# Kernel optimization log

Measured on AMD Instinct MI355X. Metric: run time of the kernel, lower is better.

## Reference

```python
import jax, jax.numpy as jnp
import numpy as np

HEADS = 4
EPS = 1e-5

def _layernorm(x, g, b):
    mu = jnp.mean(x, axis=-1, keepdims=True)
    var = jnp.var(x, axis=-1, keepdims=True)
    return (x - mu) / jnp.sqrt(var + EPS) * g + b

def setup_inputs() -> dict:
    key = jax.random.key(0)
    ks = jax.random.split(key, 16)
    N, dim, k, G = 400000, 256, 1, 4096
    h = jax.random.normal(ks[0], (N, dim), dtype=jnp.float32)
    batch = jnp.sort(jax.random.randint(ks[1], (N,), 0, G).astype(jnp.int64))
    s = 1.0 / np.sqrt(dim)
    return {
        "h": h,
        "batch": batch,
        "num_graphs": G,
        "seed": jax.random.normal(ks[2], (k, dim), dtype=jnp.float32),
        "in_proj_w": jax.random.uniform(ks[3], (3 * dim, dim), minval=-s, maxval=s, dtype=jnp.float32),
        "in_proj_b": jnp.zeros((3 * dim,), jnp.float32),
        "out_w": jax.random.uniform(ks[4], (dim, dim), minval=-s, maxval=s, dtype=jnp.float32),
        "out_b": jnp.zeros((dim,), jnp.float32),
        "w1": jax.random.uniform(ks[5], (4 * dim, dim), minval=-s, maxval=s, dtype=jnp.float32),
        "b1": jnp.zeros((4 * dim,), jnp.float32),
        "w2": jax.random.uniform(ks[6], (dim, 4 * dim), minval=-1.0 / np.sqrt(4 * dim), maxval=1.0 / np.sqrt(4 * dim), dtype=jnp.float32),
        "b2": jnp.zeros((dim,), jnp.float32),
        "g1": jnp.ones((dim,), jnp.float32),
        "beta1": jnp.zeros((dim,), jnp.float32),
        "g2": jnp.ones((dim,), jnp.float32),
        "beta2": jnp.zeros((dim,), jnp.float32),
    }

def reference(h, batch, num_graphs, seed, in_proj_w, in_proj_b, out_w, out_b,
              w1, b1, w2, b2, g1, beta1, g2, beta2):
    N, dim = h.shape
    k = seed.shape[0]
    hd = dim // HEADS
    G = num_graphs
    # q/k/v projections (torch MHA packed in_proj: rows [0:dim]=Q, [dim:2dim]=K, [2dim:]=V)
    q = seed @ in_proj_w[:dim].T + in_proj_b[:dim]                 # [k, dim]
    kk = h @ in_proj_w[dim:2 * dim].T + in_proj_b[dim:2 * dim]     # [N, dim]
    vv = h @ in_proj_w[2 * dim:].T + in_proj_b[2 * dim:]           # [N, dim]
    qh = q.reshape(k, HEADS, hd).transpose(1, 0, 2)                # [H, k, hd]
    kh = kk.reshape(N, HEADS, hd)                                  # [N, H, hd]
    vh = vv.reshape(N, HEADS, hd)                                  # [N, H, hd]
    scale = 1.0 / np.sqrt(hd)
    scores = jnp.einsum('hkd,nhd->nhk', qh, kh) * scale            # [N, H, k]
    # segment softmax over nodes of each graph
    smax = jax.ops.segment_max(scores, batch, num_segments=G)      # [G, H, k]
    e = jnp.exp(scores - smax[batch])                              # [N, H, k]
    denom = jax.ops.segment_sum(e, batch, num_segments=G)          # [G, H, k]
    wv = jax.ops.segment_sum(e[:, :, :, None] * vh[:, :, None, :], batch, num_segments=G)  # [G, H, k, hd]
    attn = jnp.where(denom[..., None] > 0, wv / jnp.maximum(denom, 1e-9)[..., None], 0.0)
    attn = attn.transpose(0, 2, 1, 3).reshape(G, k, dim)           # [G, k, dim]
    o = attn @ out_w.T + out_b                                     # [G, k, dim]
    x = _layernorm(o + seed[None, :, :], g1, beta1)
    f = jax.nn.relu(x @ w1.T + b1) @ w2.T + b2
    x = _layernorm(x + f, g2, beta2)
    # empty graphs output zeros (matches torch loop)
    count = jax.ops.segment_sum(jnp.ones((N,), jnp.float32), batch, num_segments=G)
    return jnp.where((count > 0)[:, None, None], x, 0.0)
```

## Files before the change

### kernel.cpp

```cpp
#include <hip/hip_runtime.h>
#include <hip/hip_bf16.h>


#define DIM 256
#define CHUNK 32

typedef short bf16x8 __attribute__((ext_vector_type(8)));
typedef float f32x4  __attribute__((ext_vector_type(4)));
#define MFMA16(a, b, c) __builtin_amdgcn_mfma_f32_16x16x32_bf16(a, b, c, 0, 0, 0)

#define OFF_C      0
#define OFF_D      1024
#define OFF_CONST  1040
#define OFF_P2B    2048
#define OFF_W1B    133120
#define OFF_W2B    264192
#define OFF_TB     395264
#define OFF_X1     2492416
#define OFF_X1B    3540992
#define OFF_UB     4065280
#define OFF_CNT    6162432

__global__ __launch_bounds__(256) void prep_all_kernel(
    const float* __restrict__ seed, const float* __restrict__ ipw,
    const float* __restrict__ ipb, const float* __restrict__ out_w,
    const float* __restrict__ out_b, const float* __restrict__ w1,
    const float* __restrict__ w2,
    float* __restrict__ cvec, float* __restrict__ dconst,
    float* __restrict__ constvec, __hip_bfloat16* __restrict__ P2b,
    __hip_bfloat16* __restrict__ w1b, __hip_bfloat16* __restrict__ w2b)
{
    int b = blockIdx.x, t = threadIdx.x;
    __shared__ float q_s[DIM];
    if (b < 1024) {
        int i = b >> 2, hD = b & 3;
        float a = 0.f;
        for (int j = 0; j < 64; ++j)
            a += out_w[i * DIM + hD * 64 + j]
               * ipw[(size_t)(2 * DIM + hD * 64 + j) * DIM + t];
        P2b[(size_t)i * 1024 + hD * DIM + t] = __float2bfloat16(a);
    } else if (b == 1024) {
        const float scale = 0.125f;
        float acc = ipb[t];
        for (int d = 0; d < DIM; ++d) acc += seed[d] * ipw[t * DIM + d];
        q_s[t] = acc;
        __syncthreads();
        for (int hh = 0; hh < 4; ++hh) {
            float a = 0.f;
            for (int j = 0; j < 64; ++j)
                a += q_s[hh * 64 + j] * ipw[(size_t)(DIM + hh * 64 + j) * DIM + t];
            cvec[hh * DIM + t] = a * scale;
        }
        if (t < 4) {
            float a = 0.f;
            for (int j = 0; j < 64; ++j)
                a += q_s[t * 64 + j] * ipb[DIM + t * 64 + j];
            dconst[t] = a * scale;
        }
        float cc = out_b[t];
        for (int c = 0; c < DIM; ++c)
            cc += out_w[t * DIM + c] * ipb[2 * DIM + c];
        constvec[t] = cc;
    } else if (b < 1153) {
        int base = (b - 1025) * 2048 + t;
        for (int i = 0; i < 8; ++i)
            w1b[base + i * 256] = __float2bfloat16(w1[base + i * 256]);
    } else {
        int base = (b - 1153) * 2048 + t;
        for (int i = 0; i < 8; ++i)
            w2b[base + i * 256] = __float2bfloat16(w2[base + i * 256]);
    }
}

__global__ __launch_bounds__(256) void attn_pool_kernel(
    const float* __restrict__ hmat, const int* __restrict__ batch,
    const float* __restrict__ cvec, const float* __restrict__ dconst,
    __hip_bfloat16* __restrict__ Tb, int* __restrict__ cnt, int N)
{
    int g = blockIdx.x;
    int tid = threadIdx.x;
    int lane = tid & 63, wave = tid >> 6;

    __shared__ float hbuf[CHUNK][DIM];
    __shared__ float4 esc[CHUNK];
    __shared__ float lred[4][4];

    int s, e;
    { int l = 0, r = N;
      while (l < r) { int m = (l + r) >> 1; if (batch[m] < g) l = m + 1; else r = m; }
      s = l; }
    { int l = s, r = N;
      while (l < r) { int m = (l + r) >> 1; if (batch[m] < g + 1) l = m + 1; else r = m; }
      e = l; }

    if (tid == 0) cnt[g] = e - s;
    size_t tbase = (size_t)g * 1024;
    if (e == s) {
        __hip_bfloat16 z = __float2bfloat16(0.f);
        Tb[tbase + tid] = z; Tb[tbase + 256 + tid] = z;
        Tb[tbase + 512 + tid] = z; Tb[tbase + 768 + tid] = z;
        return;
    }

    int hh = lane & 3, seg = lane >> 2;
    const float* cb = cvec + hh * DIM + seg * 16;
    float4 cr0 = *(const float4*)(cb + 0);
    float4 cr1 = *(const float4*)(cb + 4);
    float4 cr2 = *(const float4*)(cb + 8);
    float4 cr3 = *(const float4*)(cb + 12);
    float dc_mine = dconst[hh];

    float S0 = 0.f, S1 = 0.f, S2 = 0.f, S3 = 0.f;
    float lp = 0.f;

    for (int n0 = s; n0 < e; n0 += CHUNK) {
        int ccnt = min(CHUNK, e - n0);
        for (int idx = tid; idx < ccnt * 64; idx += 256) {
            int j = idx >> 6, q4 = idx & 63;
            float4 v = *(const float4*)&hmat[(size_t)(n0 + j) * DIM + q4 * 4];
            *(float4*)&hbuf[j][q4 * 4] = v;
        }
        __syncthreads();

        for (int j = wave; j < ccnt; j += 4) {
            const float* hb = &hbuf[j][seg * 16];
            float4 h0 = *(const float4*)(hb + 0);
            float4 h1 = *(const float4*)(hb + 4);
            float4 h2 = *(const float4*)(hb + 8);
            float4 h3 = *(const float4*)(hb + 12);
            float p = h0.x * cr0.x + h0.y * cr0.y + h0.z * cr0.z + h0.w * cr0.w
                    + h1.x * cr1.x + h1.y * cr1.y + h1.z * cr1.z + h1.w * cr1.w
                    + h2.x * cr2.x + h2.y * cr2.y + h2.z * cr2.z + h2.w * cr2.w
                    + h3.x * cr3.x + h3.y * cr3.y + h3.z * cr3.z + h3.w * cr3.w;
            p += __shfl_xor(p, 4);
            p += __shfl_xor(p, 8);
            p += __shfl_xor(p, 16);
            p += __shfl_xor(p, 32);
            if (lane < 4) {
                float ev = __expf(p + dc_mine);
                ((float*)&esc[j])[lane] = ev;
                lp += ev;
            }
        }
        __syncthreads();

        for (int j = 0; j < ccnt; ++j) {
            float4 e4 = esc[j];
            float hv = hbuf[j][tid];
            S0 = fmaf(e4.x, hv, S0); S1 = fmaf(e4.y, hv, S1);
            S2 = fmaf(e4.z, hv, S2); S3 = fmaf(e4.w, hv, S3);
        }
        __syncthreads();
    }

    if (lane < 4) lred[wave][lane] = lp;
    __syncthreads();
    float l0 = lred[0][0] + lred[1][0] + lred[2][0] + lred[3][0];
    float l1 = lred[0][1] + lred[1][1] + lred[2][1] + lred[3][1];
    float l2 = lred[0][2] + lred[1][2] + lred[2][2] + lred[3][2];
    float l3 = lred[0][3] + lred[1][3] + lred[2][3] + lred[3][3];
    Tb[tbase + tid]       = __float2bfloat16(S0 / l0);
    Tb[tbase + 256 + tid] = __float2bfloat16(S1 / l1);
    Tb[tbase + 512 + tid] = __float2bfloat16(S2 / l2);
    Tb[tbase + 768 + tid] = __float2bfloat16(S3 / l3);
}

__global__ __launch_bounds__(64) void gemm_o_ln1_kernel(
    const __hip_bfloat16* __restrict__ Tb, const __hip_bfloat16* __restrict__ P2b,
    const float* __restrict__ constvec, const float* __restrict__ seed,
    const float* __restrict__ g1, const float* __restrict__ be1,
    float* __restrict__ x1, __hip_bfloat16* __restrict__ x1b)
{
    int m0 = blockIdx.x * 16;
    int lane = threadIdx.x, quad = lane >> 4, l16 = lane & 15;
    f32x4 acc[16];
#pragma unroll
    for (int i = 0; i < 16; ++i) acc[i] = (f32x4){0.f, 0.f, 0.f, 0.f};
    const __hip_bfloat16* Ap = Tb + (size_t)(m0 + l16) * 1024 + quad * 8;
    const __hip_bfloat16* Bp = P2b + (size_t)l16 * 1024 + quad * 8;
    for (int k0 = 0; k0 < 1024; k0 += 32) {
        bf16x8 a = *(const bf16x8*)(Ap + k0);
#pragma unroll
        for (int nt = 0; nt < 16; ++nt) {
            bf16x8 b = *(const bf16x8*)(Bp + (size_t)nt * 16 * 1024 + k0);
            acc[nt] = MFMA16(a, b, acc[nt]);
        }
    }
    float v[16][4];
    float sum[4] = {0, 0, 0, 0}, sq[4] = {0, 0, 0, 0};
#pragma unroll
    for (int nt = 0; nt < 16; ++nt) {
        int col = nt * 16 + l16;
        float cv = constvec[col] + seed[col];
#pragma unroll
        for (int r = 0; r < 4; ++r) {
            float x = acc[nt][r] + cv;
            v[nt][r] = x; sum[r] += x; sq[r] += x * x;
        }
    }
    float mu_r[4], rs_r[4];
#pragma unroll
    for (int r = 0; r < 4; ++r) {
        float s_ = sum[r], q_ = sq[r];
        s_ += __shfl_xor(s_, 1);  q_ += __shfl_xor(q_, 1);
        s_ += __shfl_xor(s_, 2);  q_ += __shfl_xor(q_, 2);
        s_ += __shfl_xor(s_, 4);  q_ += __shfl_xor(q_, 4);
        s_ += __shfl_xor(s_, 8);  q_ += __shfl_xor(q_, 8);
        float mu = s_ * (1.f / 256);
        float var = q_ * (1.f / 256) - mu * mu;
        mu_r[r] = mu;
        rs_r[r] = rsqrtf(fmaxf(var, 0.f) + 1e-5f);
    }
#pragma unroll
    for (int nt = 0; nt < 16; ++nt) {
        int col = nt * 16 + l16;
        float gg = g1[col], bb = be1[col];
#pragma unroll
        for (int r = 0; r < 4; ++r) {
            int gr = m0 + quad * 4 + r;
            float y = (v[nt][r] - mu_r[r]) * rs_r[r] * gg + bb;
            x1[(size_t)gr * 256 + col] = y;
            x1b[(size_t)gr * 256 + col] = __float2bfloat16(y);
        }
    }
}

__global__ __launch_bounds__(64) void gemm_u_kernel(
    const __hip_bfloat16* __restrict__ x1b, const __hip_bfloat16* __restrict__ w1b,
    const float* __restrict__ b1, __hip_bfloat16* __restrict__ ub)
{
    int m0 = blockIdx.x * 16, nb0 = blockIdx.y * 128;
    int lane = threadIdx.x, quad = lane >> 4, l16 = lane & 15;
    f32x4 acc[8];
#pragma unroll
    for (int i = 0; i < 8; ++i) acc[i] = (f32x4){0.f, 0.f, 0.f, 0.f};
    const __hip_bfloat16* Ap = x1b + (size_t)(m0 + l16) * 256 + quad * 8;
    const __hip_bfloat16* Bp = w1b + (size_t)(nb0 + l16) * 256 + quad * 8;
#pragma unroll
    for (int k0 = 0; k0 < 256; k0 += 32) {
        bf16x8 a = *(const bf16x8*)(Ap + k0);
#pragma unroll
        for (int nt = 0; nt < 8; ++nt) {
            bf16x8 b = *(const bf16x8*)(Bp + (size_t)nt * 16 * 256 + k0);
            acc[nt] = MFMA16(a, b, acc[nt]);
        }
    }
#pragma unroll
    for (int nt = 0; nt < 8; ++nt) {
        int col = nb0 + nt * 16 + l16;
        float bb = b1[col];
#pragma unroll
        for (int r = 0; r < 4; ++r) {
            int gr = m0 + quad * 4 + r;
            float y = fmaxf(acc[nt][r] + bb, 0.f);
            ub[(size_t)gr * 1024 + col] = __float2bfloat16(y);
        }
    }
}

__global__ __launch_bounds__(64) void gemm_f_ln2_kernel(
    const __hip_bfloat16* __restrict__ ub, const __hip_bfloat16* __restrict__ w2b,
    const float* __restrict__ b2, const float* __restrict__ x1,
    const float* __restrict__ g2, const float* __restrict__ be2,
    const int* __restrict__ cnt, float* __restrict__ outp)
{
    int m0 = blockIdx.x * 16;
    int lane = threadIdx.x, quad = lane >> 4, l16 = lane & 15;
    f32x4 acc[16];
#pragma unroll
    for (int i = 0; i < 16; ++i) acc[i] = (f32x4){0.f, 0.f, 0.f, 0.f};
    const __hip_bfloat16* Ap = ub + (size_t)(m0 + l16) * 1024 + quad * 8;
    const __hip_bfloat16* Bp = w2b + (size_t)l16 * 1024 + quad * 8;
    for (int k0 = 0; k0 < 1024; k0 += 32) {
        bf16x8 a = *(const bf16x8*)(Ap + k0);
#pragma unroll
        for (int nt = 0; nt < 16; ++nt) {
            bf16x8 b = *(const bf16x8*)(Bp + (size_t)nt * 16 * 1024 + k0);
            acc[nt] = MFMA16(a, b, acc[nt]);
        }
    }
    float v[16][4];
    float sum[4] = {0, 0, 0, 0}, sq[4] = {0, 0, 0, 0};
#pragma unroll
    for (int nt = 0; nt < 16; ++nt) {
        int col = nt * 16 + l16;
        float bb = b2[col];
#pragma unroll
        for (int r = 0; r < 4; ++r) {
            int gr = m0 + quad * 4 + r;
            float x = acc[nt][r] + bb + x1[(size_t)gr * 256 + col];
            v[nt][r] = x; sum[r] += x; sq[r] += x * x;
        }
    }
    float mu_r[4], rs_r[4];
#pragma unroll
    for (int r = 0; r < 4; ++r) {
        float s_ = sum[r], q_ = sq[r];
        s_ += __shfl_xor(s_, 1);  q_ += __shfl_xor(q_, 1);
        s_ += __shfl_xor(s_, 2);  q_ += __shfl_xor(q_, 2);
        s_ += __shfl_xor(s_, 4);  q_ += __shfl_xor(q_, 4);
        s_ += __shfl_xor(s_, 8);  q_ += __shfl_xor(q_, 8);
        float mu = s_ * (1.f / 256);
        float var = q_ * (1.f / 256) - mu * mu;
        mu_r[r] = mu;
        rs_r[r] = rsqrtf(fmaxf(var, 0.f) + 1e-5f);
    }
#pragma unroll
    for (int r = 0; r < 4; ++r) {
        int gr = m0 + quad * 4 + r;
        float mask = (cnt[gr] > 0) ? 1.f : 0.f;
#pragma unroll
        for (int nt = 0; nt < 16; ++nt) {
            int col = nt * 16 + l16;
            float y = ((v[nt][r] - mu_r[r]) * rs_r[r] * g2[col] + be2[col]) * mask;
            outp[(size_t)gr * 256 + col] = y;
        }
    }
}

extern "C" void kernel_launch(void* const* d_in, const int* in_sizes, int n_in,
                              void* d_out, int out_size, void* d_ws, size_t ws_size,
                              hipStream_t stream) {
    const float* h     = (const float*)d_in[0];
    const int*   batch = (const int*)d_in[1];
    const float* seed  = (const float*)d_in[3];
    const float* ipw   = (const float*)d_in[4];
    const float* ipb   = (const float*)d_in[5];
    const float* out_w = (const float*)d_in[6];
    const float* out_b = (const float*)d_in[7];
    const float* w1    = (const float*)d_in[8];
    const float* b1    = (const float*)d_in[9];
    const float* w2    = (const float*)d_in[10];
    const float* b2    = (const float*)d_in[11];
    const float* g1    = (const float*)d_in[12];
    const float* be1   = (const float*)d_in[13];
    const float* g2    = (const float*)d_in[14];
    const float* be2   = (const float*)d_in[15];

    int N = in_sizes[1];
    int G = out_size / DIM;

    float* ws = (float*)d_ws;
    float* cvec     = ws + OFF_C;
    float* dconst   = ws + OFF_D;
    float* constvec = ws + OFF_CONST;
    __hip_bfloat16* P2b = (__hip_bfloat16*)(ws + OFF_P2B);
    __hip_bfloat16* w1b = (__hip_bfloat16*)(ws + OFF_W1B);
    __hip_bfloat16* w2b = (__hip_bfloat16*)(ws + OFF_W2B);
    __hip_bfloat16* Tb  = (__hip_bfloat16*)(ws + OFF_TB);
    float* x1       = ws + OFF_X1;
    __hip_bfloat16* x1b = (__hip_bfloat16*)(ws + OFF_X1B);
    __hip_bfloat16* ub  = (__hip_bfloat16*)(ws + OFF_UB);
    int*   cnt      = (int*)(ws + OFF_CNT);

    prep_all_kernel<<<1281, 256, 0, stream>>>(seed, ipw, ipb, out_w, out_b, w1, w2,
                                              cvec, dconst, constvec, P2b, w1b, w2b);
    attn_pool_kernel<<<G, 256, 0, stream>>>(h, batch, cvec, dconst, Tb, cnt, N);
    gemm_o_ln1_kernel<<<G / 16, 64, 0, stream>>>(Tb, P2b, constvec, seed, g1, be1,
                                                 x1, x1b);
    gemm_u_kernel<<<dim3(G / 16, 8), 64, 0, stream>>>(x1b, w1b, b1, ub);
    gemm_f_ln2_kernel<<<G / 16, 64, 0, stream>>>(ub, w2b, b2, x1, g2, be2, cnt,
                                                 (float*)d_out);
}
```

Baseline: 713.8 us.

## Fuse out-proj/LN1, FFN up and down/LN2 into one kernel; register-prefetch h chunks

Three post-attention GEMM kernels are merged into one 256-thread kernel per 16-graph tile. Intermediates x1 and the FFN hidden activations stay in shared memory instead of global, and LayerNorm statistics are reduced across the four waves through LDS. Separately, the attention pooling kernel now prefetches the next chunk of h into registers while the current chunk is processed, overlapping global loads with compute. This adds register pressure and more shared memory, and the fused GEMMs run with fewer blocks (G/16) than the old grid for the up-projection.

```diff
diff --git a/kernel.cpp b/kernel.cpp
--- a/kernel.cpp
+++ b/kernel.cpp
@@ -16,9 +16,6 @@
 #define OFF_W1B    133120
 #define OFF_W2B    264192
 #define OFF_TB     395264
-#define OFF_X1     2492416
-#define OFF_X1B    3540992
-#define OFF_UB     4065280
 #define OFF_CNT    6162432
 
 __global__ __launch_bounds__(256) void prep_all_kernel(
@@ -113,14 +110,43 @@
     float S0 = 0.f, S1 = 0.f, S2 = 0.f, S3 = 0.f;
     float lp = 0.f;
 
+    float4 rbuf[8];
+    {
+        int cc0 = min(CHUNK, e - s);
+#pragma unroll
+        for (int i = 0; i < 8; ++i) {
+            int idx = tid + i * 256;
+            if (idx < cc0 * 64) {
+                int j = idx >> 6, q4 = idx & 63;
+                rbuf[i] = *(const float4*)&hmat[(size_t)(s + j) * DIM + q4 * 4];
+            }
+        }
+    }
+
     for (int n0 = s; n0 < e; n0 += CHUNK) {
         int ccnt = min(CHUNK, e - n0);
-        for (int idx = tid; idx < ccnt * 64; idx += 256) {
-            int j = idx >> 6, q4 = idx & 63;
-            float4 v = *(const float4*)&hmat[(size_t)(n0 + j) * DIM + q4 * 4];
-            *(float4*)&hbuf[j][q4 * 4] = v;
+#pragma unroll
+        for (int i = 0; i < 8; ++i) {
+            int idx = tid + i * 256;
+            if (idx < ccnt * 64) {
+                int j = idx >> 6, q4 = idx & 63;
+                *(float4*)&hbuf[j][q4 * 4] = rbuf[i];
+            }
         }
         __syncthreads();
+
+        int n1 = n0 + CHUNK;
+        if (n1 < e) {
+            int cn = min(CHUNK, e - n1);
+#pragma unroll
+            for (int i = 0; i < 8; ++i) {
+                int idx = tid + i * 256;
+                if (idx < cn * 64) {
+                    int j = idx >> 6, q4 = idx & 63;
+                    rbuf[i] = *(const float4*)&hmat[(size_t)(n1 + j) * DIM + q4 * 4];
+                }
+            }
+        }
 
         for (int j = wave; j < ccnt; j += 4) {
             const float* hb = &hbuf[j][seg * 16];
@@ -165,155 +191,167 @@
     Tb[tbase + 768 + tid] = __float2bfloat16(S3 / l3);
 }
 
-__global__ __launch_bounds__(64) void gemm_o_ln1_kernel(
+__global__ __launch_bounds__(256) void mlp_fused_kernel(
     const __hip_bfloat16* __restrict__ Tb, const __hip_bfloat16* __restrict__ P2b,
     const float* __restrict__ constvec, const float* __restrict__ seed,
     const float* __restrict__ g1, const float* __restrict__ be1,
-    float* __restrict__ x1, __hip_bfloat16* __restrict__ x1b)
-{
-    int m0 = blockIdx.x * 16;
-    int lane = threadIdx.x, quad = lane >> 4, l16 = lane & 15;
-    f32x4 acc[16];
-#pragma unroll
-    for (int i = 0; i < 16; ++i) acc[i] = (f32x4){0.f, 0.f, 0.f, 0.f};
-    const __hip_bfloat16* Ap = Tb + (size_t)(m0 + l16) * 1024 + quad * 8;
-    const __hip_bfloat16* Bp = P2b + (size_t)l16 * 1024 + quad * 8;
-    for (int k0 = 0; k0 < 1024; k0 += 32) {
-        bf16x8 a = *(const bf16x8*)(Ap + k0);
-#pragma unroll
-        for (int nt = 0; nt < 16; ++nt) {
-            bf16x8 b = *(const bf16x8*)(Bp + (size_t)nt * 16 * 1024 + k0);
-            acc[nt] = MFMA16(a, b, acc[nt]);
-        }
-    }
-    float v[16][4];
-    float sum[4] = {0, 0, 0, 0}, sq[4] = {0, 0, 0, 0};
-#pragma unroll
-    for (int nt = 0; nt < 16; ++nt) {
-        int col = nt * 16 + l16;
-        float cv = constvec[col] + seed[col];
-#pragma unroll
-        for (int r = 0; r < 4; ++r) {
-            float x = acc[nt][r] + cv;
-            v[nt][r] = x; sum[r] += x; sq[r] += x * x;
-        }
-    }
-    float mu_r[4], rs_r[4];
-#pragma unroll
-    for (int r = 0; r < 4; ++r) {
-        float s_ = sum[r], q_ = sq[r];
-        s_ += __shfl_xor(s_, 1);  q_ += __shfl_xor(q_, 1);
-        s_ += __shfl_xor(s_, 2);  q_ += __shfl_xor(q_, 2);
-        s_ += __shfl_xor(s_, 4);  q_ += __shfl_xor(q_, 4);
-        s_ += __shfl_xor(s_, 8);  q_ += __shfl_xor(q_, 8);
-        float mu = s_ * (1.f / 256);
-        float var = q_ * (1.f / 256) - mu * mu;
-        mu_r[r] = mu;
-        rs_r[r] = rsqrtf(fmaxf(var, 0.f) + 1e-5f);
-    }
-#pragma unroll
-    for (int nt = 0; nt < 16; ++nt) {
-        int col = nt * 16 + l16;
-        float gg = g1[col], bb = be1[col];
-#pragma unroll
-        for (int r = 0; r < 4; ++r) {
-            int gr = m0 + quad * 4 + r;
-            float y = (v[nt][r] - mu_r[r]) * rs_r[r] * gg + bb;
-            x1[(size_t)gr * 256 + col] = y;
-            x1b[(size_t)gr * 256 + col] = __float2bfloat16(y);
-        }
-    }
-}
-
-__global__ __launch_bounds__(64) void gemm_u_kernel(
-    const __hip_bfloat16* __restrict__ x1b, const __hip_bfloat16* __restrict__ w1b,
-    const float* __restrict__ b1, __hip_bfloat16* __restrict__ ub)
-{
-    int m0 = blockIdx.x * 16, nb0 = blockIdx.y * 128;
-    int lane = threadIdx.x, quad = lane >> 4, l16 = lane & 15;
-    f32x4 acc[8];
-#pragma unroll
-    for (int i = 0; i < 8; ++i) acc[i] = (f32x4){0.f, 0.f, 0.f, 0.f};
-    const __hip_bfloat16* Ap = x1b + (size_t)(m0 + l16) * 256 + quad * 8;
-    const __hip_bfloat16* Bp = w1b + (size_t)(nb0 + l16) * 256 + quad * 8;
-#pragma unroll
-    for (int k0 = 0; k0 < 256; k0 += 32) {
-        bf16x8 a = *(const bf16x8*)(Ap + k0);
-#pragma unroll
-        for (int nt = 0; nt < 8; ++nt) {
-            bf16x8 b = *(const bf16x8*)(Bp + (size_t)nt * 16 * 256 + k0);
-            acc[nt] = MFMA16(a, b, acc[nt]);
-        }
-    }
-#pragma unroll
-    for (int nt = 0; nt < 8; ++nt) {
-        int col = nb0 + nt * 16 + l16;
-        float bb = b1[col];
-#pragma unroll
-        for (int r = 0; r < 4; ++r) {
-            int gr = m0 + quad * 4 + r;
-            float y = fmaxf(acc[nt][r] + bb, 0.f);
-            ub[(size_t)gr * 1024 + col] = __float2bfloat16(y);
-        }
-    }
-}
-
-__global__ __launch_bounds__(64) void gemm_f_ln2_kernel(
-    const __hip_bfloat16* __restrict__ ub, const __hip_bfloat16* __restrict__ w2b,
-    const float* __restrict__ b2, const float* __restrict__ x1,
+    const __hip_bfloat16* __restrict__ w1b, const float* __restrict__ b1,
+    const __hip_bfloat16* __restrict__ w2b, const float* __restrict__ b2,
     const float* __restrict__ g2, const float* __restrict__ be2,
     const int* __restrict__ cnt, float* __restrict__ outp)
 {
     int m0 = blockIdx.x * 16;
-    int lane = threadIdx.x, quad = lane >> 4, l16 = lane & 15;
-    f32x4 acc[16];
-#pragma unroll
-    for (int i = 0; i < 16; ++i) acc[i] = (f32x4){0.f, 0.f, 0.f, 0.f};
-    const __hip_bfloat16* Ap = ub + (size_t)(m0 + l16) * 1024 + quad * 8;
-    const __hip_bfloat16* Bp = w2b + (size_t)l16 * 1024 + quad * 8;
+    int tid = threadIdx.x;
+    int w = tid >> 6, lane = tid & 63, quad = lane >> 4, l16 = lane & 15;
+
+    __shared__ float x1s[16][260];
+    __shared__ __hip_bfloat16 x1bs[16][264];
+    __shared__ __hip_bfloat16 us[16][1032];
+    __shared__ float redS[4][16], redQ[4][16];
+
+    f32x4 acc0[4];
+#pragma unroll
+    for (int i = 0; i < 4; ++i) acc0[i] = (f32x4){0.f, 0.f, 0.f, 0.f};
+    const __hip_bfloat16* Ap0 = Tb + (size_t)(m0 + l16) * 1024 + quad * 8;
+    const __hip_bfloat16* Bp0 = P2b + (size_t)(w * 64 + l16) * 1024 + quad * 8;
     for (int k0 = 0; k0 < 1024; k0 += 32) {
-        bf16x8 a = *(const bf16x8*)(Ap + k0);
+        bf16x8 a = *(const bf16x8*)(Ap0 + k0);
+#pragma unroll
+        for (int nt = 0; nt < 4; ++nt) {
+            bf16x8 b = *(const bf16x8*)(Bp0 + (size_t)nt * 16 * 1024 + k0);
+            acc0[nt] = MFMA16(a, b, acc0[nt]);
+        }
+    }
+    float v0[4][4];
+    {
+        float sum[4] = {0, 0, 0, 0}, sq[4] = {0, 0, 0, 0};
+#pragma unroll
+        for (int nt = 0; nt < 4; ++nt) {
+            int col = w * 64 + nt * 16 + l16;
+            float cv = constvec[col] + seed[col];
+#pragma unroll
+            for (int r = 0; r < 4; ++r) {
+                float x = acc0[nt][r] + cv;
+                v0[nt][r] = x; sum[r] += x; sq[r] += x * x;
+            }
+        }
+#pragma unroll
+        for (int r = 0; r < 4; ++r) {
+            float s_ = sum[r], q_ = sq[r];
+            s_ += __shfl_xor(s_, 1);  q_ += __shfl_xor(q_, 1);
+            s_ += __shfl_xor(s_, 2);  q_ += __shfl_xor(q_, 2);
+            s_ += __shfl_xor(s_, 4);  q_ += __shfl_xor(q_, 4);
+            s_ += __shfl_xor(s_, 8);  q_ += __shfl_xor(q_, 8);
+            if (l16 == 0) { redS[w][quad * 4 + r] = s_; redQ[w][quad * 4 + r] = q_; }
+        }
+    }
+    __syncthreads();
+    {
+        float mu_r[4], rs_r[4];
+#pragma unroll
+        for (int r = 0; r < 4; ++r) {
+            int row = quad * 4 + r;
+            float s_ = redS[0][row] + redS[1][row] + redS[2][row] + redS[3][row];
+            float q_ = redQ[0][row] + redQ[1][row] + redQ[2][row] + redQ[3][row];
+            float mu = s_ * (1.f / 256);
+            float var = q_ * (1.f / 256) - mu * mu;
+            mu_r[r] = mu;
+            rs_r[r] = rsqrtf(fmaxf(var, 0.f) + 1e-5f);
+        }
+#pragma unroll
+        for (int nt = 0; nt < 4; ++nt) {
+            int col = w * 64 + nt * 16 + l16;
+            float gg = g1[col], bb = be1[col];
+#pragma unroll
+            for (int r = 0; r < 4; ++r) {
+                int row = quad * 4 + r;
+                float y = (v0[nt][r] - mu_r[r]) * rs_r[r] * gg + bb;
+                x1s[row][col] = y;
+                x1bs[row][col] = __float2bfloat16(y);
+            }
+        }
+    }
+    __syncthreads();
+
+    f32x4 acc1[16];
+#pragma unroll
+    for (int i = 0; i < 16; ++i) acc1[i] = (f32x4){0.f, 0.f, 0.f, 0.f};
+    const __hip_bfloat16* Bp1 = w1b + (size_t)(w * 256 + l16) * 256 + quad * 8;
+#pragma unroll
+    for (int k0 = 0; k0 < 256; k0 += 32) {
+        bf16x8 a = *(const bf16x8*)&x1bs[l16][quad * 8 + k0];
 #pragma unroll
         for (int nt = 0; nt < 16; ++nt) {
-            bf16x8 b = *(const bf16x8*)(Bp + (size_t)nt * 16 * 1024 + k0);
-            acc[nt] = MFMA16(a, b, acc[nt]);
-        }
-    }
-    float v[16][4];
-    float sum[4] = {0, 0, 0, 0}, sq[4] = {0, 0, 0, 0};
+            bf16x8 b = *(const bf16x8*)(Bp1 + (size_t)nt * 16 * 256 + k0);
+            acc1[nt] = MFMA16(a, b, acc1[nt]);
+        }
+    }
 #pragma unroll
     for (int nt = 0; nt < 16; ++nt) {
-        int col = nt * 16 + l16;
-        float bb = b2[col];
-#pragma unroll
-        for (int r = 0; r < 4; ++r) {
-            int gr = m0 + quad * 4 + r;
-            float x = acc[nt][r] + bb + x1[(size_t)gr * 256 + col];
-            v[nt][r] = x; sum[r] += x; sq[r] += x * x;
-        }
-    }
-    float mu_r[4], rs_r[4];
-#pragma unroll
-    for (int r = 0; r < 4; ++r) {
-        float s_ = sum[r], q_ = sq[r];
-        s_ += __shfl_xor(s_, 1);  q_ += __shfl_xor(q_, 1);
-        s_ += __shfl_xor(s_, 2);  q_ += __shfl_xor(q_, 2);
-        s_ += __shfl_xor(s_, 4);  q_ += __shfl_xor(q_, 4);
-        s_ += __shfl_xor(s_, 8);  q_ += __shfl_xor(q_, 8);
-        float mu = s_ * (1.f / 256);
-        float var = q_ * (1.f / 256) - mu * mu;
-        mu_r[r] = mu;
-        rs_r[r] = rsqrtf(fmaxf(var, 0.f) + 1e-5f);
-    }
-#pragma unroll
-    for (int r = 0; r < 4; ++r) {
-        int gr = m0 + quad * 4 + r;
-        float mask = (cnt[gr] > 0) ? 1.f : 0.f;
-#pragma unroll
-        for (int nt = 0; nt < 16; ++nt) {
-            int col = nt * 16 + l16;
-            float y = ((v[nt][r] - mu_r[r]) * rs_r[r] * g2[col] + be2[col]) * mask;
-            outp[(size_t)gr * 256 + col] = y;
+        int col = w * 256 + nt * 16 + l16;
+        float bb = b1[col];
+#pragma unroll
+        for (int r = 0; r < 4; ++r) {
+            int row = quad * 4 + r;
+            us[row][col] = __float2bfloat16(fmaxf(acc1[nt][r] + bb, 0.f));
+        }
+    }
+    __syncthreads();
+
+    f32x4 acc2[4];
+#pragma unroll
+    for (int i = 0; i < 4; ++i) acc2[i] = (f32x4){0.f, 0.f, 0.f, 0.f};
+    const __hip_bfloat16* Bp2 = w2b + (size_t)(w * 64 + l16) * 1024 + quad * 8;
+    for (int k0 = 0; k0 < 1024; k0 += 32) {
+        bf16x8 a = *(const bf16x8*)&us[l16][quad * 8 + k0];
+#pragma unroll
+        for (int nt = 0; nt < 4; ++nt) {
+            bf16x8 b = *(const bf16x8*)(Bp2 + (size_t)nt * 16 * 1024 + k0);
+            acc2[nt] = MFMA16(a, b, acc2[nt]);
+        }
+    }
+    float v2[4][4];
+    {
+        float sum[4] = {0, 0, 0, 0}, sq[4] = {0, 0, 0, 0};
+#pragma unroll
+        for (int nt = 0; nt < 4; ++nt) {
+            int col = w * 64 + nt * 16 + l16;
+            float bb = b2[col];
+#pragma unroll
+            for (int r = 0; r < 4; ++r) {
+                int row = quad * 4 + r;
+                float x = acc2[nt][r] + bb + x1s[row][col];
+                v2[nt][r] = x; sum[r] += x; sq[r] += x * x;
+            }
+        }
+#pragma unroll
+        for (int r = 0; r < 4; ++r) {
+            float s_ = sum[r], q_ = sq[r];
+            s_ += __shfl_xor(s_, 1);  q_ += __shfl_xor(q_, 1);
+            s_ += __shfl_xor(s_, 2);  q_ += __shfl_xor(q_, 2);
+            s_ += __shfl_xor(s_, 4);  q_ += __shfl_xor(q_, 4);
+            s_ += __shfl_xor(s_, 8);  q_ += __shfl_xor(q_, 8);
+            if (l16 == 0) { redS[w][quad * 4 + r] = s_; redQ[w][quad * 4 + r] = q_; }
+        }
+    }
+    __syncthreads();
+    {
+#pragma unroll
+        for (int r = 0; r < 4; ++r) {
+            int row = quad * 4 + r;
+            float s_ = redS[0][row] + redS[1][row] + redS[2][row] + redS[3][row];
+            float q_ = redQ[0][row] + redQ[1][row] + redQ[2][row] + redQ[3][row];
+            float mu = s_ * (1.f / 256);
+            float var = q_ * (1.f / 256) - mu * mu;
+            float rs = rsqrtf(fmaxf(var, 0.f) + 1e-5f);
+            int gr = m0 + row;
+            float mask = (cnt[gr] > 0) ? 1.f : 0.f;
+#pragma unroll
+            for (int nt = 0; nt < 4; ++nt) {
+                int col = w * 64 + nt * 16 + l16;
+                float y = ((v2[nt][r] - mu) * rs * g2[col] + be2[col]) * mask;
+                outp[(size_t)gr * 256 + col] = y;
+            }
         }
     }
 }
@@ -348,17 +386,12 @@
     __hip_bfloat16* w1b = (__hip_bfloat16*)(ws + OFF_W1B);
     __hip_bfloat16* w2b = (__hip_bfloat16*)(ws + OFF_W2B);
     __hip_bfloat16* Tb  = (__hip_bfloat16*)(ws + OFF_TB);
-    float* x1       = ws + OFF_X1;
-    __hip_bfloat16* x1b = (__hip_bfloat16*)(ws + OFF_X1B);
-    __hip_bfloat16* ub  = (__hip_bfloat16*)(ws + OFF_UB);
     int*   cnt      = (int*)(ws + OFF_CNT);
 
     prep_all_kernel<<<1281, 256, 0, stream>>>(seed, ipw, ipb, out_w, out_b, w1, w2,
                                               cvec, dconst, constvec, P2b, w1b, w2b);
     attn_pool_kernel<<<G, 256, 0, stream>>>(h, batch, cvec, dconst, Tb, cnt, N);
-    gemm_o_ln1_kernel<<<G / 16, 64, 0, stream>>>(Tb, P2b, constvec, seed, g1, be1,
-                                                 x1, x1b);
-    gemm_u_kernel<<<dim3(G / 16, 8), 64, 0, stream>>>(x1b, w1b, b1, ub);
-    gemm_f_ln2_kernel<<<G / 16, 64, 0, stream>>>(ub, w2b, b2, x1, g2, be2, cnt,
+    mlp_fused_kernel<<<G / 16, 256, 0, stream>>>(Tb, P2b, constvec, seed, g1, be1,
+                                                 w1b, b1, w2b, b2, g2, be2, cnt,
                                                  (float*)d_out);
 }
```

After: 808.9 us. +13.3%, slower.
